# Performance work log

Hardware: AMD Instinct MI355X
Metric: run time of the kernel (lower is better)

## Reference

```python
import jax, jax.numpy as jnp
import numpy as np

N_TOK, D_MODEL, N_EXPERTS, TOP_K = 8192, 512, 8, 2


def setup_inputs() -> dict:
    key = jax.random.key(0)
    k1, k2, k3 = jax.random.split(key, 3)
    x = jax.random.normal(k1, (N_TOK, D_MODEL), jnp.float32)
    w_gate = jax.random.normal(k2, (D_MODEL, N_EXPERTS), jnp.float32) * 0.02
    expert_w = jax.random.normal(k3, (N_EXPERTS, D_MODEL, D_MODEL), jnp.float32) * (D_MODEL ** -0.5)
    return {"x": x, "w_gate": w_gate, "expert_w": expert_w, "top_k": TOP_K}


def _cv_sq(v):
    m = jnp.mean(v)
    return jnp.var(v) / (m * m + 1e-10)


def reference(x, w_gate, expert_w, top_k):
    # ---- Gate (clean top-k gating, eval mode of noisy-top-k) ----
    logits = x @ w_gate                              # [N, E]
    top_vals, top_idx = jax.lax.top_k(logits, top_k)  # [N, k]
    top_gates = jax.nn.softmax(top_vals, axis=-1)
    n, e = logits.shape
    gates = jnp.zeros((n, e), x.dtype).at[jnp.arange(n)[:, None], top_idx].set(top_gates)

    # ---- dispatch -> per-expert GEMM -> log-domain combine ----
    # combine(): stitched = cat(expert_out).exp() * nonzero_gates; index_add over
    # batch index; zeros -> eps; log. Dense-equivalent (tokens with gate 0
    # contribute exactly nothing):
    expert_out = jnp.einsum('nd,edf->nef', x, expert_w)   # per-expert outputs [N, E, D]
    combined = jnp.einsum('ne,nef->nf', gates, jnp.exp(expert_out))  # [N, D]
    eps = np.float32(np.finfo(np.float64).eps)
    combined = jnp.where(combined == 0, eps, combined)
    out = jnp.log(combined)

    # ---- load-balance aux loss: cv^2(importance) + cv^2(load) ----
    importance = gates.sum(0)
    load = (gates > 0).sum(0).astype(x.dtype)
    balance_loss = _cv_sq(importance) + _cv_sq(load)
    return out, balance_loss
```

## Files before the change

### kernel.cpp

```cpp
#include <hip/hip_runtime.h>
#include <hip/hip_bf16.h>
#include <math.h>

#define N_TOK 8192
#define D 512
#define NE 8

typedef float f32x4 __attribute__((ext_vector_type(4)));
typedef __bf16 bf16x8 __attribute__((ext_vector_type(8)));
typedef unsigned short u16;

#define OFF_TOKE  256
#define OFF_TOKG  65792
#define OFF_BUCK  131328
#define OFF_XB    (1u << 20)
#define OFF_EWT   (OFF_XB + 8u * 1024 * 1024)
#define OFF_Y     (OFF_EWT + 4u * 1024 * 1024)

__device__ __forceinline__ u16 f2b(float v) {
    __hip_bfloat16 h = __float2bfloat16(v);
    return *reinterpret_cast<u16*>(&h);
}
__device__ __forceinline__ float b2f(u16 u) {
    __hip_bfloat16 h;
    *reinterpret_cast<u16*>(&h) = u;
    return __bfloat162float(h);
}

typedef __attribute__((address_space(1))) const void* gp1_t;
typedef __attribute__((address_space(3))) void* lp3_t;
__device__ __forceinline__ void gload16(const void* g, void* l) {
    __builtin_amdgcn_global_load_lds((gp1_t)g, (lp3_t)l, 16, 0, 0);
}

__global__ __launch_bounds__(256) void gate_kernel(
    const float* __restrict__ x, const float* __restrict__ wg,
    int* __restrict__ tok_e, float* __restrict__ tok_g, u16* __restrict__ xb)
{
    __shared__ float wgs[NE * D];
    for (int i = threadIdx.x; i < NE * D; i += 256) {
        int d = i >> 3, e = i & 7;
        wgs[e * D + d] = wg[i];
    }
    __syncthreads();

    int wave = threadIdx.x >> 6, lane = threadIdx.x & 63;
    int n = blockIdx.x * 4 + wave;
    const float* xr = x + (size_t)n * D;
    u16* xbr = xb + (size_t)n * D;

    float p[NE];
#pragma unroll
    for (int e = 0; e < NE; ++e) p[e] = 0.f;
#pragma unroll
    for (int it = 0; it < 8; ++it) {
        float xv = xr[it * 64 + lane];
        xbr[it * 64 + lane] = f2b(xv);
#pragma unroll
        for (int e = 0; e < NE; ++e)
            p[e] += xv * wgs[e * D + it * 64 + lane];
    }
#pragma unroll
    for (int off = 32; off > 0; off >>= 1) {
#pragma unroll
        for (int e = 0; e < NE; ++e)
            p[e] += __shfl_xor(p[e], off);
    }

    if (lane == 0) {
        int e1 = 0; float v1 = p[0];
#pragma unroll
        for (int e = 1; e < NE; ++e) if (p[e] > v1) { v1 = p[e]; e1 = e; }
        int e2 = -1; float v2 = -INFINITY;
#pragma unroll
        for (int e = 0; e < NE; ++e) if (e != e1 && p[e] > v2) { v2 = p[e]; e2 = e; }
        float t = __expf(v2 - v1);
        float inv = 1.f / (1.f + t);
        tok_e[2 * n] = e1;     tok_e[2 * n + 1] = e2;
        tok_g[2 * n] = inv;    tok_g[2 * n + 1] = t * inv;
    }
}

__global__ __launch_bounds__(256) void bucketize_kernel(
    const int* __restrict__ tok_e, const float* __restrict__ tok_g,
    int* __restrict__ count, float* __restrict__ imp, int* __restrict__ bucket)
{
    __shared__ int lcnt[NE], lbase[NE];
    __shared__ float limp[NE];
    int tid = threadIdx.x;
    if (tid < NE) { lcnt[tid] = 0; limp[tid] = 0.f; }
    __syncthreads();

    int n = blockIdx.x * 256 + tid;
    int e1 = tok_e[2 * n], e2 = tok_e[2 * n + 1];
    float g1 = tok_g[2 * n], g2 = tok_g[2 * n + 1];
    int o1 = atomicAdd(&lcnt[e1], 1);
    int o2 = atomicAdd(&lcnt[e2], 1);
    atomicAdd(&limp[e1], g1);
    atomicAdd(&limp[e2], g2);
    __syncthreads();
    if (tid < NE) {
        lbase[tid] = atomicAdd(&count[tid], lcnt[tid]);
        atomicAdd(&imp[tid], limp[tid]);
    }
    __syncthreads();
    bucket[e1 * N_TOK + lbase[e1] + o1] = 2 * n;
    bucket[e2 * N_TOK + lbase[e2] + o2] = 2 * n + 1;
}

__global__ __launch_bounds__(256) void prep_w_kernel(
    const float* __restrict__ ew, u16* __restrict__ ewt)
{
    __shared__ float tile[64][65];
    int b = blockIdx.x;
    int e = b >> 6, dt = (b >> 3) & 7, ftl = b & 7;
    int t = threadIdx.x;
    int c = t & 63, rq = t >> 6;
    const float* src = ew + (size_t)e * D * D + (size_t)(dt * 64) * D + ftl * 64;
#pragma unroll
    for (int i = 0; i < 16; ++i) {
        int r = i * 4 + rq;
        tile[r][c] = src[(size_t)r * D + c];
    }
    __syncthreads();
    u16* dst = ewt + (size_t)e * D * D + (size_t)(ftl * 64) * D + dt * 64;
#pragma unroll
    for (int i = 0; i < 16; ++i) {
        int f = i * 4 + rq;
        dst[(size_t)f * D + c] = f2b(tile[c][f]);
    }
}

__global__ __launch_bounds__(256) void moe_gemm(
    const u16* __restrict__ xb, const u16* __restrict__ ewt,
    const int* __restrict__ count, const int* __restrict__ bucket,
    u16* __restrict__ y)
{
    int b = blockIdx.x;
    int ft = b & 3;
    int tt = (b >> 2) & 63;
    int e  = b >> 8;
    int cnt = count[e];
    if (tt * 128 >= cnt) return;

    __shared__ int sl[128];
    __shared__ __align__(16) u16 As[128 * 32];
    __shared__ __align__(16) u16 Bs[128 * 32];

    int tid = threadIdx.x;
    if (tid < 128) {
        int idx = tt * 128 + tid;
        sl[tid] = (idx < cnt) ? bucket[e * N_TOK + idx] : -1;
    }
    __syncthreads();

    int w = tid >> 6, l = tid & 63;
    int c8 = (l & 3) * 8;
    int r0 = w * 32 + (l >> 2);
    int r1 = r0 + 16;
    int s0 = sl[r0], s1 = sl[r1];
    int ta0 = (s0 < 0) ? 0 : (s0 >> 1);
    int ta1 = (s1 < 0) ? 0 : (s1 >> 1);
    const u16* gA0 = xb + (size_t)ta0 * D + c8;
    const u16* gA1 = xb + (size_t)ta1 * D + c8;
    const u16* gB0 = ewt + ((size_t)e * D + ft * 128 + r0) * D + c8;
    const u16* gB1 = ewt + ((size_t)e * D + ft * 128 + r1) * D + c8;
    u16* lA0 = &As[(w * 32) * 32];
    u16* lA1 = &As[(w * 32 + 16) * 32];
    u16* lB0 = &Bs[(w * 32) * 32];
    u16* lB1 = &Bs[(w * 32 + 16) * 32];

    int wm = w & 1, wn = w >> 1;
    int lm = l & 15, kq = (l >> 4) * 8;

    f32x4 acc[4][4] = {};

    for (int kc = 0; kc < 16; ++kc) {
        __syncthreads();
        gload16(gA0 + kc * 32, lA0);
        gload16(gA1 + kc * 32, lA1);
        gload16(gB0 + kc * 32, lB0);
        gload16(gB1 + kc * 32, lB1);
        __syncthreads();

        bf16x8 af[4], bfv[4];
#pragma unroll
        for (int i = 0; i < 4; ++i)
            af[i] = *(const bf16x8*)&As[(wm * 64 + i * 16 + lm) * 32 + kq];
#pragma unroll
        for (int j = 0; j < 4; ++j)
            bfv[j] = *(const bf16x8*)&Bs[(wn * 64 + j * 16 + lm) * 32 + kq];
#pragma unroll
        for (int i = 0; i < 4; ++i)
#pragma unroll
            for (int j = 0; j < 4; ++j)
                acc[i][j] = __builtin_amdgcn_mfma_f32_16x16x32_bf16(
                    af[i], bfv[j], acc[i][j], 0, 0, 0);
    }

    int quad = l >> 4;
#pragma unroll
    for (int i = 0; i < 4; ++i) {
        int mbase = wm * 64 + i * 16 + quad * 4;
#pragma unroll
        for (int r = 0; r < 4; ++r) {
            int s = sl[mbase + r];
            if (s < 0) continue;
            u16* dst = y + (size_t)s * D + ft * 128 + wn * 64 + lm;
#pragma unroll
            for (int j = 0; j < 4; ++j)
                dst[j * 16] = f2b(acc[i][j][r]);
        }
    }
}

__global__ __launch_bounds__(256) void combine_kernel(
    const u16* __restrict__ y, const float* __restrict__ tok_g,
    float* __restrict__ out)
{
    int idx = blockIdx.x * 256 + threadIdx.x;
    int n = idx >> 7;
    int c = (idx & 127) * 4;
    const ushort4 ua = *(const ushort4*)(y + (size_t)(2 * n) * D + c);
    const ushort4 ub = *(const ushort4*)(y + (size_t)(2 * n + 1) * D + c);
    float g1 = tok_g[2 * n], g2 = tok_g[2 * n + 1];
    const float eps = 2.2204460492503131e-16f;
    float4 r;
    float v;
    v = g1 * __expf(b2f(ua.x)) + g2 * __expf(b2f(ub.x)); r.x = __logf(v == 0.f ? eps : v);
    v = g1 * __expf(b2f(ua.y)) + g2 * __expf(b2f(ub.y)); r.y = __logf(v == 0.f ? eps : v);
    v = g1 * __expf(b2f(ua.z)) + g2 * __expf(b2f(ub.z)); r.z = __logf(v == 0.f ? eps : v);
    v = g1 * __expf(b2f(ua.w)) + g2 * __expf(b2f(ub.w)); r.w = __logf(v == 0.f ? eps : v);
    *(float4*)(out + (size_t)n * D + c) = r;
}

__global__ void loss_kernel(const int* __restrict__ count,
                            const float* __restrict__ imp,
                            float* __restrict__ out)
{
    if (threadIdx.x == 0 && blockIdx.x == 0) {
        float mi = 0.f, ml = 0.f;
        for (int e = 0; e < NE; ++e) { mi += imp[e]; ml += (float)count[e]; }
        mi *= 0.125f; ml *= 0.125f;
        float vi = 0.f, vl = 0.f;
        for (int e = 0; e < NE; ++e) {
            float di = imp[e] - mi;          vi += di * di;
            float dl = (float)count[e] - ml; vl += dl * dl;
        }
        vi *= 0.125f; vl *= 0.125f;
        out[N_TOK * D] = vi / (mi * mi + 1e-10f) + vl / (ml * ml + 1e-10f);
    }
}

extern "C" void kernel_launch(void* const* d_in, const int* in_sizes, int n_in,
                              void* d_out, int out_size, void* d_ws, size_t ws_size,
                              hipStream_t stream)
{
    const float* x  = (const float*)d_in[0];
    const float* wg = (const float*)d_in[1];
    const float* ew = (const float*)d_in[2];
    char* ws = (char*)d_ws;
    int*   count  = (int*)(ws + 0);
    float* imp    = (float*)(ws + 64);
    int*   tok_e  = (int*)(ws + OFF_TOKE);
    float* tok_g  = (float*)(ws + OFF_TOKG);
    int*   bucket = (int*)(ws + OFF_BUCK);
    u16*   xb     = (u16*)(ws + OFF_XB);
    u16*   ewt    = (u16*)(ws + OFF_EWT);
    u16*   y      = (u16*)(ws + OFF_Y);
    float* out    = (float*)d_out;

    hipMemsetAsync(ws, 0, 128, stream);
    gate_kernel<<<N_TOK / 4, 256, 0, stream>>>(x, wg, tok_e, tok_g, xb);
    prep_w_kernel<<<NE * 64, 256, 0, stream>>>(ew, ewt);
    bucketize_kernel<<<N_TOK / 256, 256, 0, stream>>>(tok_e, tok_g, count, imp, bucket);
    moe_gemm<<<NE * 64 * 4, 256, 0, stream>>>(xb, ewt, count, bucket, y);
    combine_kernel<<<(N_TOK * D / 4) / 256, 256, 0, stream>>>(y, tok_g, out);
    loss_kernel<<<1, 64, 0, stream>>>(count, imp, out);
}
```

Measured before the change: 122.2 us.

## Merge gate/weight-prep and combine/loss launches; stage GEMM epilogue through LDS

Folds the weight transpose-convert blocks into the gate kernel's grid and the loss computation into an extra block of the combine kernel, cutting two kernel launches. The GEMM epilogue now writes accumulators to shared memory and then emits 16-byte vectorized rows to y instead of scattered 2-byte stores. This adds an extra sync and LDS traffic in the epilogue, and the merged gate kernel uses a larger shared buffer, which may lower occupancy.

```diff
diff --git a/kernel.cpp b/kernel.cpp
--- a/kernel.cpp
+++ b/kernel.cpp
@@ -9,6 +9,7 @@
 typedef float f32x4 __attribute__((ext_vector_type(4)));
 typedef __bf16 bf16x8 __attribute__((ext_vector_type(8)));
 typedef unsigned short u16;
+typedef u16 u16x8 __attribute__((ext_vector_type(8)));
 
 #define OFF_TOKE  256
 #define OFF_TOKG  65792
@@ -33,19 +34,46 @@
     __builtin_amdgcn_global_load_lds((gp1_t)g, (lp3_t)l, 16, 0, 0);
 }
 
-__global__ __launch_bounds__(256) void gate_kernel(
+__global__ __launch_bounds__(256) void gate_prep_kernel(
     const float* __restrict__ x, const float* __restrict__ wg,
-    int* __restrict__ tok_e, float* __restrict__ tok_g, u16* __restrict__ xb)
-{
-    __shared__ float wgs[NE * D];
-    for (int i = threadIdx.x; i < NE * D; i += 256) {
+    const float* __restrict__ ew,
+    int* __restrict__ tok_e, float* __restrict__ tok_g, u16* __restrict__ xb,
+    u16* __restrict__ ewt)
+{
+    __shared__ __align__(16) float sbuf[64 * 65];
+    int b = blockIdx.x;
+    int tid = threadIdx.x;
+
+    if (b >= 2048) {
+        int pb = b - 2048;
+        float (*tile)[65] = (float(*)[65])sbuf;
+        int e = pb >> 6, dt = (pb >> 3) & 7, ftl = pb & 7;
+        int c = tid & 63, rq = tid >> 6;
+        const float* src = ew + (size_t)e * D * D + (size_t)(dt * 64) * D + ftl * 64;
+#pragma unroll
+        for (int i = 0; i < 16; ++i) {
+            int r = i * 4 + rq;
+            tile[r][c] = src[(size_t)r * D + c];
+        }
+        __syncthreads();
+        u16* dst = ewt + (size_t)e * D * D + (size_t)(ftl * 64) * D + dt * 64;
+#pragma unroll
+        for (int i = 0; i < 16; ++i) {
+            int f = i * 4 + rq;
+            dst[(size_t)f * D + c] = f2b(tile[c][f]);
+        }
+        return;
+    }
+
+    float* wgs = sbuf;
+    for (int i = tid; i < NE * D; i += 256) {
         int d = i >> 3, e = i & 7;
         wgs[e * D + d] = wg[i];
     }
     __syncthreads();
 
-    int wave = threadIdx.x >> 6, lane = threadIdx.x & 63;
-    int n = blockIdx.x * 4 + wave;
+    int wave = tid >> 6, lane = tid & 63;
+    int n = b * 4 + wave;
     const float* xr = x + (size_t)n * D;
     u16* xbr = xb + (size_t)n * D;
 
@@ -108,29 +136,6 @@
     bucket[e2 * N_TOK + lbase[e2] + o2] = 2 * n + 1;
 }
 
-__global__ __launch_bounds__(256) void prep_w_kernel(
-    const float* __restrict__ ew, u16* __restrict__ ewt)
-{
-    __shared__ float tile[64][65];
-    int b = blockIdx.x;
-    int e = b >> 6, dt = (b >> 3) & 7, ftl = b & 7;
-    int t = threadIdx.x;
-    int c = t & 63, rq = t >> 6;
-    const float* src = ew + (size_t)e * D * D + (size_t)(dt * 64) * D + ftl * 64;
-#pragma unroll
-    for (int i = 0; i < 16; ++i) {
-        int r = i * 4 + rq;
-        tile[r][c] = src[(size_t)r * D + c];
-    }
-    __syncthreads();
-    u16* dst = ewt + (size_t)e * D * D + (size_t)(ftl * 64) * D + dt * 64;
-#pragma unroll
-    for (int i = 0; i < 16; ++i) {
-        int f = i * 4 + rq;
-        dst[(size_t)f * D + c] = f2b(tile[c][f]);
-    }
-}
-
 __global__ __launch_bounds__(256) void moe_gemm(
     const u16* __restrict__ xb, const u16* __restrict__ ewt,
     const int* __restrict__ count, const int* __restrict__ bucket,
@@ -144,8 +149,9 @@
     if (tt * 128 >= cnt) return;
 
     __shared__ int sl[128];
-    __shared__ __align__(16) u16 As[128 * 32];
-    __shared__ __align__(16) u16 Bs[128 * 32];
+    __shared__ __align__(16) u16 smem[16384];
+    u16* As = smem;
+    u16* Bs = smem + 8192;
 
     int tid = threadIdx.x;
     if (tid < 128) {
@@ -171,7 +177,7 @@
     u16* lB1 = &Bs[(w * 32 + 16) * 32];
 
     int wm = w & 1, wn = w >> 1;
-    int lm = l & 15, kq = (l >> 4) * 8;
+    int lm = l & 15, quad = l >> 4, kq = quad * 8;
 
     f32x4 acc[4][4] = {};
 
@@ -198,26 +204,52 @@
                     af[i], bfv[j], acc[i][j], 0, 0, 0);
     }
 
-    int quad = l >> 4;
-#pragma unroll
-    for (int i = 0; i < 4; ++i) {
-        int mbase = wm * 64 + i * 16 + quad * 4;
-#pragma unroll
-        for (int r = 0; r < 4; ++r) {
-            int s = sl[mbase + r];
-            if (s < 0) continue;
-            u16* dst = y + (size_t)s * D + ft * 128 + wn * 64 + lm;
+    __syncthreads();
+    u16* Es = smem + w * 2304;
+#pragma unroll
+    for (int h = 0; h < 2; ++h) {
+#pragma unroll
+        for (int i2 = 0; i2 < 2; ++i2) {
+            int i = h * 2 + i2;
 #pragma unroll
             for (int j = 0; j < 4; ++j)
-                dst[j * 16] = f2b(acc[i][j][r]);
+#pragma unroll
+                for (int r = 0; r < 4; ++r)
+                    Es[(i2 * 16 + quad * 4 + r) * 72 + j * 16 + lm] =
+                        f2b(acc[i][j][r]);
+        }
+        int row = l >> 1, hc = l & 1;
+        int s = sl[wm * 64 + h * 32 + row];
+        const u16* src = Es + row * 72 + hc * 32;
+        u16* dst = y + (size_t)((s < 0) ? 0 : s) * D + ft * 128 + wn * 64 + hc * 32;
+        if (s >= 0) {
+#pragma unroll
+            for (int c = 0; c < 4; ++c)
+                *(u16x8*)(dst + c * 8) = *(const u16x8*)(src + c * 8);
         }
     }
 }
 
 __global__ __launch_bounds__(256) void combine_kernel(
     const u16* __restrict__ y, const float* __restrict__ tok_g,
+    const int* __restrict__ count, const float* __restrict__ imp,
     float* __restrict__ out)
 {
+    if (blockIdx.x == 4096) {
+        if (threadIdx.x == 0) {
+            float mi = 0.f, ml = 0.f;
+            for (int e = 0; e < NE; ++e) { mi += imp[e]; ml += (float)count[e]; }
+            mi *= 0.125f; ml *= 0.125f;
+            float vi = 0.f, vl = 0.f;
+            for (int e = 0; e < NE; ++e) {
+                float di = imp[e] - mi;          vi += di * di;
+                float dl = (float)count[e] - ml; vl += dl * dl;
+            }
+            vi *= 0.125f; vl *= 0.125f;
+            out[N_TOK * D] = vi / (mi * mi + 1e-10f) + vl / (ml * ml + 1e-10f);
+        }
+        return;
+    }
     int idx = blockIdx.x * 256 + threadIdx.x;
     int n = idx >> 7;
     int c = (idx & 127) * 4;
@@ -234,24 +266,6 @@
     *(float4*)(out + (size_t)n * D + c) = r;
 }
 
-__global__ void loss_kernel(const int* __restrict__ count,
-                            const float* __restrict__ imp,
-                            float* __restrict__ out)
-{
-    if (threadIdx.x == 0 && blockIdx.x == 0) {
-        float mi = 0.f, ml = 0.f;
-        for (int e = 0; e < NE; ++e) { mi += imp[e]; ml += (float)count[e]; }
-        mi *= 0.125f; ml *= 0.125f;
-        float vi = 0.f, vl = 0.f;
-        for (int e = 0; e < NE; ++e) {
-            float di = imp[e] - mi;          vi += di * di;
-            float dl = (float)count[e] - ml; vl += dl * dl;
-        }
-        vi *= 0.125f; vl *= 0.125f;
-        out[N_TOK * D] = vi / (mi * mi + 1e-10f) + vl / (ml * ml + 1e-10f);
-    }
-}
-
 extern "C" void kernel_launch(void* const* d_in, const int* in_sizes, int n_in,
                               void* d_out, int out_size, void* d_ws, size_t ws_size,
                               hipStream_t stream)
@@ -271,10 +285,8 @@
     float* out    = (float*)d_out;
 
     hipMemsetAsync(ws, 0, 128, stream);
-    gate_kernel<<<N_TOK / 4, 256, 0, stream>>>(x, wg, tok_e, tok_g, xb);
-    prep_w_kernel<<<NE * 64, 256, 0, stream>>>(ew, ewt);
+    gate_prep_kernel<<<2048 + 512, 256, 0, stream>>>(x, wg, ew, tok_e, tok_g, xb, ewt);
     bucketize_kernel<<<N_TOK / 256, 256, 0, stream>>>(tok_e, tok_g, count, imp, bucket);
     moe_gemm<<<NE * 64 * 4, 256, 0, stream>>>(xb, ewt, count, bucket, y);
-    combine_kernel<<<(N_TOK * D / 4) / 256, 256, 0, stream>>>(y, tok_g, out);
-    loss_kernel<<<1, 64, 0, stream>>>(count, imp, out);
-}
+    combine_kernel<<<4097, 256, 0, stream>>>(y, tok_g, count, imp, out);
+}
```

New measurement: 120.4 us. No clear change (-1.5%).
